# Performance work log

Hardware: AMD Instinct MI355X
Metric: run time of the kernel (lower is better)

The kernel has to match this reference:

```python
import jax, jax.numpy as jnp
import numpy as np

V, E, D_LAT, NC, L = 30000, 256, 256, 10, 4096
B = 8
D_IN = 2 * D_LAT   # mamba expand=2 -> 512
N_ST = 16          # d_state
DT_R = 16          # dt_rank = ceil(d_model/16)
D_CONV = 4


def conv1d(x, w, b, pad, groups=1):
    # x: [B,C,L], w: [O, C//groups, K] (torch layout)
    y = jax.lax.conv_general_dilated(x, w, (1,), [(pad[0], pad[1])],
                                     dimension_numbers=('NCH', 'OIH', 'NCH'),
                                     feature_group_count=groups)
    return y + b[None, :, None]


def setup_inputs() -> dict:
    key = jax.random.key(0)
    ks = jax.random.split(key, 12)
    nrm = lambda k, s, sc=0.02: (jax.random.normal(k, s) * sc).astype(jnp.float32)
    return {
        'tokens': jax.random.randint(ks[0], (B, L), 0, V),
        'emb': nrm(ks[1], (V, E)),
        'conv1_w': nrm(ks[2], (128, E, 5)), 'conv1_b': jnp.zeros((128,), jnp.float32),
        'conv2_w': nrm(ks[3], (D_LAT, 128, 3)), 'conv2_b': jnp.zeros((D_LAT,), jnp.float32),
        'in_proj_w': nrm(ks[4], (2 * D_IN, D_LAT)),
        'convdw_w': nrm(ks[5], (D_IN, 1, D_CONV), 0.2), 'convdw_b': jnp.zeros((D_IN,), jnp.float32),
        'x_proj_w': nrm(ks[6], (DT_R + 2 * N_ST, D_IN)),
        'dt_proj_w': nrm(ks[7], (D_IN, DT_R), 0.1),
        'dt_proj_b': jnp.full((D_IN,), -4.0, jnp.float32),  # softplus^-1 of small dt
        'A_log': jnp.broadcast_to(jnp.log(jnp.arange(1, N_ST + 1, dtype=jnp.float32)), (D_IN, N_ST)) + jnp.zeros((D_IN, N_ST), jnp.float32),
        'Dp': jnp.ones((D_IN,), jnp.float32),
        'out_proj_w': nrm(ks[8], (D_LAT, D_IN)),
        'fc_w': nrm(ks[9], (NC, D_LAT)), 'fc_b': jnp.zeros((NC,), jnp.float32),
    }


def mamba_block(u, in_proj_w, convdw_w, convdw_b, x_proj_w, dt_proj_w, dt_proj_b, A_log, Dp, out_proj_w):
    # u: [B, Lm, d_model]
    Bsz = u.shape[0]
    xz = u @ in_proj_w.T                              # [B,Lm,2*Din]
    x, z = jnp.split(xz, 2, axis=-1)
    # causal depthwise conv (torch pads both sides, slices [:L] == left-pad only)
    xc = conv1d(x.transpose(0, 2, 1), convdw_w, convdw_b, (D_CONV - 1, 0), groups=D_IN)
    x = jax.nn.silu(xc.transpose(0, 2, 1))            # [B,Lm,Din]
    dbc = x @ x_proj_w.T                              # [B,Lm,dt_rank+2N]
    dt, Bm, Cm = jnp.split(dbc, [DT_R, DT_R + N_ST], axis=-1)
    dt = jax.nn.softplus(dt @ dt_proj_w.T + dt_proj_b)  # [B,Lm,Din]
    A = -jnp.exp(A_log)                               # [Din,N]

    def step(h, inp):
        dt_t, B_t, C_t, x_t = inp                     # [B,Din],[B,N],[B,N],[B,Din]
        dA = jnp.exp(dt_t[..., None] * A)             # [B,Din,N]
        h = h * dA + (dt_t * x_t)[..., None] * B_t[:, None, :]
        y = jnp.einsum('bdn,bn->bd', h, C_t)
        return h, y

    h0 = jnp.zeros((Bsz, D_IN, N_ST), u.dtype)
    xs = (dt.transpose(1, 0, 2), Bm.transpose(1, 0, 2), Cm.transpose(1, 0, 2), x.transpose(1, 0, 2))
    _, ys = jax.lax.scan(step, h0, xs)                # [Lm,B,Din]
    y = ys.transpose(1, 0, 2) + x * Dp
    y = y * jax.nn.silu(z)
    return y @ out_proj_w.T                           # [B,Lm,d_model]


def reference(tokens, emb, conv1_w, conv1_b, conv2_w, conv2_b, in_proj_w, convdw_w, convdw_b,
              x_proj_w, dt_proj_w, dt_proj_b, A_log, Dp, out_proj_w, fc_w, fc_b):
    x = emb[tokens]                                   # [B,L,E]
    x = x.transpose(0, 2, 1)                          # [B,E,L]
    x = jax.nn.relu(conv1d(x, conv1_w, conv1_b, (2, 2)))
    b, c, l = x.shape
    x = x.reshape(b, c, l // 2, 2).max(-1)            # MaxPool1d(2)
    x = jax.nn.relu(conv1d(x, conv2_w, conv2_b, (1, 1)))
    x = x.transpose(0, 2, 1)                          # [B,L/2,latent]
    x = mamba_block(x, in_proj_w, convdw_w, convdw_b, x_proj_w, dt_proj_w, dt_proj_b, A_log, Dp, out_proj_w)
    x = x.mean(axis=1)                                # [B,latent]
    return x @ fc_w.T + fc_b                          # [B,num_classes]
```

## Files before the change

### kernel.cpp

```cpp
#include <hip/hip_runtime.h>
#include <hip/hip_bf16.h>

constexpr int Bn   = 8;
constexpr int L    = 4096;
constexpr int E    = 256;
constexpr int Lh   = 2048;
constexpr int C1n  = 128;
constexpr int Dlat = 256;
constexpr int Din  = 512;
constexpr int Nst  = 16;
constexpr int M2   = Bn * Lh;
constexpr int NCH  = 64;
constexpr int TC   = 32;

constexpr long o_wtx   = 0;
constexpr long o_wtdt  = o_wtx  + 512L*48;
constexpr long o_bf    = o_wtdt + 16L*512;
constexpr long o_xeb   = o_bf    + 524288/2;
constexpr long o_out1b = o_xeb   + (8L*4100*256)/2;
constexpr long o_ub    = o_out1b + (8L*2050*128)/2;
constexpr long o_xz    = o_ub    + (16384L*256)/2;
constexpr long o_xbuf  = o_xz    + 16384L*1024;
constexpr long o_dbc   = o_xbuf  + 16384L*512;
constexpr long o_dt    = o_dbc   + 16384L*48;
constexpr long o_hend  = o_dt    + 16384L*512;
constexpr long o_P     = o_hend  + 8L*512*NCH*16;
constexpr long o_hin   = o_P     + 8L*512*NCH*16;
constexpr long o_ym    = o_hin   + 8L*512*NCH*16;

typedef __attribute__((ext_vector_type(8))) short bf8_t;
typedef __attribute__((ext_vector_type(4))) float f4_t;

__device__ inline short f2bf(float f) {
    unsigned int u = __float_as_uint(f);
    unsigned int r = (u + 0x7FFFu + ((u >> 16) & 1u)) >> 16;
    return (short)r;
}

__global__ void k_prep(const float* __restrict__ w1, const float* __restrict__ w2,
                       const float* __restrict__ win, const float* __restrict__ xw,
                       const float* __restrict__ dtw, float* __restrict__ ws) {
    int idx = blockIdx.x * 256 + threadIdx.x;
    if (idx < 24576) {
        int n_ = idx % 48; int k = idx / 48;
        ws[o_wtx + idx] = xw[n_*512 + k];
    } else if (idx < 32768) {
        int j = idx - 24576;
        int n_ = j & 511; int k = j >> 9;
        ws[o_wtdt + j] = dtw[n_*16 + k];
    } else if (idx < 557056) {
        int j = idx - 32768;
        short* wsS = (short*)(ws + o_bf);
        if (j < 163840) {
            int n_ = j / 1280; int r = j - n_*1280; int s = r >> 8; int c = r & 255;
            wsS[j] = f2bf(w1[(n_*256 + c)*5 + s]);
        } else if (j < 262144) {
            int jj = j - 163840;
            int n_ = jj / 384; int r = jj - n_*384; int s = r >> 7; int c = r & 127;
            wsS[j] = f2bf(w2[(n_*128 + c)*3 + s]);
        } else {
            int jj = j - 262144;
            int n_ = jj >> 8; int k = jj & 255;
            wsS[j] = f2bf(win[n_*256 + k]);
        }
    }
}

__global__ void k_embed(const int* __restrict__ tok, const float* __restrict__ emb,
                        short* __restrict__ xeb) {
    int idx = blockIdx.x * 256 + threadIdx.x;
    int r = idx >> 5;
    int c8 = (idx & 31) << 3;
    int b = r / 4100; int tr = r - b*4100;
    bf8_t v = {0,0,0,0,0,0,0,0};
    if (tr >= 2 && tr < 4098) {
        int t = tok[b*4096 + tr - 2];
        const float* e = emb + (long)t*256 + c8;
        #pragma unroll
        for (int i = 0; i < 8; ++i) v[i] = f2bf(e[i]);
    }
    *(bf8_t*)&xeb[(long)r*256 + c8] = v;
}

__global__ void k_zpad(short* __restrict__ out1b) {
    int i = threadIdx.x;
    for (int j = i; j < 2048; j += 256) {
        int b = j >> 8; int rsel = (j >> 7) & 1; int c = j & 127;
        long row = (long)b*2050 + (rsel ? 2049 : 0);
        out1b[row*128 + c] = 0;
    }
}

template<int SHIFTS, int TPS, int EPI>
__global__ __launch_bounds__(256) void k_mgemm(const short* __restrict__ A, int ars, long batchA,
                                               const short* __restrict__ Bt, int ktot,
                                               const float* __restrict__ bias,
                                               short* __restrict__ outB, float* __restrict__ outF,
                                               int ors, long batchOut) {
    constexpr int KT = SHIFTS * TPS;
    constexpr int C  = TPS * 64;
    __shared__ short As[2][64][68];
    __shared__ short Bs[2][128][68];
    int tid = threadIdx.x;
    int l = tid & 63, w = tid >> 6;
    int m0 = blockIdx.x * 64;
    int n0 = blockIdx.y * 128;
    long zA = (long)blockIdx.z * batchA;
    long zO = (long)blockIdx.z * batchOut;

    bf8_t aReg[2], bReg[4];

    auto gload = [&](int kt) {
        int s = kt / TPS, c0 = (kt % TPS) * 64;
        const short* Ab = A + zA + (long)(m0 + s) * ars + c0;
        #pragma unroll
        for (int j = 0; j < 2; ++j) {
            int idx = tid + j*256;
            int r = idx >> 3, cc = (idx & 7) * 8;
            aReg[j] = *(const bf8_t*)&Ab[(long)r * ars + cc];
        }
        const short* Bb = Bt + (long)n0 * ktot + s * C + c0;
        #pragma unroll
        for (int j = 0; j < 4; ++j) {
            int idx = tid + j*256;
            int r = idx >> 3, cc = (idx & 7) * 8;
            bReg[j] = *(const bf8_t*)&Bb[(long)r * ktot + cc];
        }
    };
    auto lwrite = [&](int buf) {
        #pragma unroll
        for (int j = 0; j < 2; ++j) {
            int idx = tid + j*256;
            int r = idx >> 3, cc = (idx & 7) * 8;
            *(bf8_t*)&As[buf][r][cc] = aReg[j];
        }
        #pragma unroll
        for (int j = 0; j < 4; ++j) {
            int idx = tid + j*256;
            int r = idx >> 3, cc = (idx & 7) * 8;
            *(bf8_t*)&Bs[buf][r][cc] = bReg[j];
        }
    };

    f4_t acc[4][2];
    #pragma unroll
    for (int m = 0; m < 4; ++m)
        #pragma unroll
        for (int n = 0; n < 2; ++n) acc[m][n] = (f4_t){0.f, 0.f, 0.f, 0.f};

    gload(0);
    lwrite(0);
    __syncthreads();
    for (int kt = 0; kt < KT; ++kt) {
        int buf = kt & 1;
        if (kt + 1 < KT) gload(kt + 1);
        #pragma unroll
        for (int ks = 0; ks < 2; ++ks) {
            int kk = ks*32 + ((l >> 4) << 3);
            bf8_t a[4], b[2];
            #pragma unroll
            for (int m = 0; m < 4; ++m)
                a[m] = *(const bf8_t*)&As[buf][m*16 + (l & 15)][kk];
            #pragma unroll
            for (int n = 0; n < 2; ++n)
                b[n] = *(const bf8_t*)&Bs[buf][w*32 + n*16 + (l & 15)][kk];
            #pragma unroll
            for (int m = 0; m < 4; ++m)
                #pragma unroll
                for (int n = 0; n < 2; ++n)
                    acc[m][n] = __builtin_amdgcn_mfma_f32_16x16x32_bf16(a[m], b[n], acc[m][n], 0, 0, 0);
        }
        if (kt + 1 < KT) {
            lwrite(buf ^ 1);
            __syncthreads();
        }
    }

    #pragma unroll
    for (int mt = 0; mt < 4; ++mt)
        #pragma unroll
        for (int nt = 0; nt < 2; ++nt) {
            f4_t c = acc[mt][nt];
            int col = n0 + w*32 + nt*16 + (l & 15);
            int r0 = m0 + mt*16 + ((l >> 4) << 2);
            if constexpr (EPI == 0) {
                #pragma unroll
                for (int j = 0; j < 4; ++j)
                    outF[zO + (long)(r0 + j) * ors + col] = c[j];
            } else if constexpr (EPI == 1) {
                float bv = bias[col];
                #pragma unroll
                for (int j = 0; j < 4; ++j)
                    outB[zO + (long)(r0 + j) * ors + col] = f2bf(fmaxf(c[j] + bv, 0.f));
            } else {
                float bv = bias[col];
                float p0 = fmaxf(fmaxf(c[0], c[1]) + bv, 0.f);
                float p1 = fmaxf(fmaxf(c[2], c[3]) + bv, 0.f);
                int tp = r0 >> 1;
                outB[zO + (long)(tp + 1) * ors + col] = f2bf(p0);
                outB[zO + (long)(tp + 2) * ors + col] = f2bf(p1);
            }
        }
}

template<int ACT>
__global__ __launch_bounds__(256) void k_gemm(const float* __restrict__ A, int lda,
                                              const float* __restrict__ WT,
                                              const float* __restrict__ bias,
                                              float* __restrict__ out,
                                              int M, int N, int K) {
    __shared__ float As[16][68];
    __shared__ float Bs[16][64];
    int n0 = blockIdx.x * 64, m0 = blockIdx.y * 64;
    int tid = threadIdx.x;
    int ti = tid >> 4, tj = tid & 15;
    float acc[4][4] = {};
    for (int k0 = 0; k0 < K; k0 += 16) {
        {
            int mm = tid >> 2, kq = tid & 3;
            float4 v = *(const float4*)&A[(long)(m0 + mm)*lda + k0 + kq*4];
            As[kq*4+0][mm] = v.x; As[kq*4+1][mm] = v.y;
            As[kq*4+2][mm] = v.z; As[kq*4+3][mm] = v.w;
        }
        {
            int kk = tid >> 4, n4 = tid & 15;
            float4 v = {0.f,0.f,0.f,0.f};
            if (n0 + n4*4 < N)
                v = *(const float4*)&WT[(long)(k0 + kk)*N + n0 + n4*4];
            *(float4*)&Bs[kk][n4*4] = v;
        }
        __syncthreads();
        #pragma unroll
        for (int kk = 0; kk < 16; ++kk) {
            float4 av = *(float4*)&As[kk][ti*4];
            float4 bv = *(float4*)&Bs[kk][tj*4];
            acc[0][0] += av.x*bv.x; acc[0][1] += av.x*bv.y; acc[0][2] += av.x*bv.z; acc[0][3] += av.x*bv.w;
            acc[1][0] += av.y*bv.x; acc[1][1] += av.y*bv.y; acc[1][2] += av.y*bv.z; acc[1][3] += av.y*bv.w;
            acc[2][0] += av.z*bv.x; acc[2][1] += av.z*bv.y; acc[2][2] += av.z*bv.z; acc[2][3] += av.z*bv.w;
            acc[3][0] += av.w*bv.x; acc[3][1] += av.w*bv.y; acc[3][2] += av.w*bv.z; acc[3][3] += av.w*bv.w;
        }
        __syncthreads();
    }
    if (n0 + tj*4 >= N) return;
    float4 bv = {0.f,0.f,0.f,0.f};
    if (bias) bv = *(const float4*)&bias[n0 + tj*4];
    #pragma unroll
    for (int i = 0; i < 4; ++i) {
        int m = m0 + ti*4 + i;
        float4 v;
        v.x = acc[i][0] + bv.x; v.y = acc[i][1] + bv.y;
        v.z = acc[i][2] + bv.z; v.w = acc[i][3] + bv.w;
        if (ACT == 1) {
            v.x = (v.x > 20.f) ? v.x : log1pf(__expf(v.x));
            v.y = (v.y > 20.f) ? v.y : log1pf(__expf(v.y));
            v.z = (v.z > 20.f) ? v.z : log1pf(__expf(v.z));
            v.w = (v.w > 20.f) ? v.w : log1pf(__expf(v.w));
        }
        *(float4*)&out[(long)m*N + n0 + tj*4] = v;
    }
}

__global__ void k_dwconv(const float* __restrict__ xz, const float* __restrict__ wdw,
                         const float* __restrict__ bdw, float* __restrict__ xout) {
    int idx = blockIdx.x * 256 + threadIdx.x;
    int d4 = idx & 127; int rem = idx >> 7;
    int t = rem & 2047; int b = rem >> 11;
    int d0 = d4 * 4;
    float4 acc = *(const float4*)&bdw[d0];
    #pragma unroll
    for (int k = 0; k < 4; ++k) {
        int tt = t - 3 + k;
        if (tt >= 0) {
            float4 v = *(const float4*)&xz[((long)(b*Lh + tt))*1024 + d0];
            acc.x += v.x * wdw[(d0+0)*4 + k];
            acc.y += v.y * wdw[(d0+1)*4 + k];
            acc.z += v.z * wdw[(d0+2)*4 + k];
            acc.w += v.w * wdw[(d0+3)*4 + k];
        }
    }
    acc.x = acc.x / (1.f + __expf(-acc.x));
    acc.y = acc.y / (1.f + __expf(-acc.y));
    acc.z = acc.z / (1.f + __expf(-acc.z));
    acc.w = acc.w / (1.f + __expf(-acc.w));
    *(float4*)&xout[(long)idx * 4] = acc;
}

__global__ __launch_bounds__(256) void k_scan_a(const float* __restrict__ dt,
                                                const float* __restrict__ x,
                                                const float* __restrict__ dbc,
                                                const float* __restrict__ A_log,
                                                float* __restrict__ hend,
                                                float* __restrict__ Pbuf) {
    __shared__ float4 Bs4[TC][4];
    int c = blockIdx.x;
    int b = blockIdx.z;
    int tid = threadIdx.x;
    int d = blockIdx.y * 256 + tid;
    for (int i = tid; i < TC*4; i += 256) {
        int tt = i >> 2, q = i & 3;
        Bs4[tt][q] = *(const float4*)&dbc[((long)b*Lh + c*TC + tt)*48 + 16 + q*4];
    }
    __syncthreads();
    float A_[16];
    #pragma unroll
    for (int n = 0; n < 16; ++n) A_[n] = -__expf(A_log[d*16 + n]);
    float h[16];
    #pragma unroll
    for (int n = 0; n < 16; ++n) h[n] = 0.f;
    float sd = 0.f;
    long base = ((long)b*Lh + c*TC)*512 + d;
    #pragma unroll 4
    for (int tt = 0; tt < TC; ++tt) {
        float dtv = dt[base + (long)tt*512];
        float xv  = x[base + (long)tt*512];
        float u = dtv * xv;
        sd += dtv;
        float Bv[16];
        *(float4*)&Bv[0]  = Bs4[tt][0]; *(float4*)&Bv[4]  = Bs4[tt][1];
        *(float4*)&Bv[8]  = Bs4[tt][2]; *(float4*)&Bv[12] = Bs4[tt][3];
        #pragma unroll
        for (int n = 0; n < 16; ++n) {
            float dA = __expf(dtv * A_[n]);
            h[n] = h[n] * dA + u * Bv[n];
        }
    }
    long o = (((long)b*Din + d)*NCH + c)*16;
    #pragma unroll
    for (int n = 0; n < 16; ++n) hend[o + n] = h[n];
    #pragma unroll
    for (int n = 0; n < 16; ++n) Pbuf[o + n] = __expf(A_[n] * sd);
}

__global__ void k_scan_b(const float* __restrict__ hend, const float* __restrict__ Pbuf,
                         float* __restrict__ hin) {
    int idx = blockIdx.x * 256 + threadIdx.x;
    int n = idx & 15; long bd = idx >> 4;
    long base = bd * NCH * 16 + n;
    float h = 0.f;
    for (int c = 0; c < NCH; ++c) {
        hin[base + c*16] = h;
        h = hend[base + c*16] + Pbuf[base + c*16] * h;
    }
}

__global__ __launch_bounds__(256) void k_scan_c(const float* __restrict__ dt,
                                                const float* __restrict__ x,
                                                const float* __restrict__ xz,
                                                const float* __restrict__ dbc,
                                                const float* __restrict__ A_log,
                                                const float* __restrict__ Dp,
                                                const float* __restrict__ hin,
                                                float* __restrict__ ym) {
    __shared__ float4 Bs4[TC][4], Cs4[TC][4];
    int c = blockIdx.x;
    int b = blockIdx.z;
    int tid = threadIdx.x;
    int d = blockIdx.y * 256 + tid;
    for (int i = tid; i < TC*4; i += 256) {
        int tt = i >> 2, q = i & 3;
        long rb = ((long)b*Lh + c*TC + tt)*48;
        Bs4[tt][q] = *(const float4*)&dbc[rb + 16 + q*4];
        Cs4[tt][q] = *(const float4*)&dbc[rb + 32 + q*4];
    }
    __syncthreads();
    float A_[16];
    #pragma unroll
    for (int n = 0; n < 16; ++n) A_[n] = -__expf(A_log[d*16 + n]);
    float h[16];
    long o = (((long)b*Din + d)*NCH + c)*16;
    #pragma unroll
    for (int n = 0; n < 16; ++n) h[n] = hin[o + n];
    float Dpv = Dp[d];
    float ysum = 0.f;
    long base = ((long)b*Lh + c*TC)*512 + d;
    long zbase = ((long)b*Lh + c*TC)*1024 + 512 + d;
    #pragma unroll 2
    for (int tt = 0; tt < TC; ++tt) {
        float dtv = dt[base + (long)tt*512];
        float xv  = x[base + (long)tt*512];
        float zv  = xz[zbase + (long)tt*1024];
        float u = dtv * xv;
        float Bv[16], Cv[16];
        *(float4*)&Bv[0]  = Bs4[tt][0]; *(float4*)&Bv[4]  = Bs4[tt][1];
        *(float4*)&Bv[8]  = Bs4[tt][2]; *(float4*)&Bv[12] = Bs4[tt][3];
        *(float4*)&Cv[0]  = Cs4[tt][0]; *(float4*)&Cv[4]  = Cs4[tt][1];
        *(float4*)&Cv[8]  = Cs4[tt][2]; *(float4*)&Cv[12] = Cs4[tt][3];
        float p = 0.f;
        #pragma unroll
        for (int n = 0; n < 16; ++n) {
            float dA = __expf(dtv * A_[n]);
            h[n] = h[n] * dA + u * Bv[n];
            p += h[n] * Cv[n];
        }
        float sz = zv / (1.f + __expf(-zv));
        ysum += (p + xv * Dpv) * sz;
    }
    atomicAdd(&ym[b*Din + d], ysum);
}

__global__ void k_tail(const float* __restrict__ ym, const float* __restrict__ ow,
                       const float* __restrict__ fcw, const float* __restrict__ fcb,
                       float* __restrict__ out) {
    __shared__ float yls[512];
    __shared__ float xs[256];
    int b = blockIdx.x, c = threadIdx.x;
    yls[c] = ym[b*512 + c];
    yls[c + 256] = ym[b*512 + 256 + c];
    __syncthreads();
    float s = 0.f;
    for (int d = 0; d < 512; ++d) s += yls[d] * ow[c*512 + d];
    xs[c] = s * (1.f / 2048.f);
    __syncthreads();
    if (c < 10) {
        float t = fcb[c];
        for (int k = 0; k < 256; ++k) t += xs[k] * fcw[c*256 + k];
        out[b*10 + c] = t;
    }
}

extern "C" void kernel_launch(void* const* d_in, const int* in_sizes, int n_in,
                              void* d_out, int out_size, void* d_ws, size_t ws_size,
                              hipStream_t stream) {
    const int*   tok  = (const int*)d_in[0];
    const float* emb  = (const float*)d_in[1];
    const float* w1   = (const float*)d_in[2];
    const float* b1   = (const float*)d_in[3];
    const float* w2   = (const float*)d_in[4];
    const float* b2   = (const float*)d_in[5];
    const float* win  = (const float*)d_in[6];
    const float* wdw  = (const float*)d_in[7];
    const float* bdw  = (const float*)d_in[8];
    const float* xw   = (const float*)d_in[9];
    const float* dtw  = (const float*)d_in[10];
    const float* dtb  = (const float*)d_in[11];
    const float* alog = (const float*)d_in[12];
    const float* Dp   = (const float*)d_in[13];
    const float* ow   = (const float*)d_in[14];
    const float* fcw  = (const float*)d_in[15];
    const float* fcb  = (const float*)d_in[16];
    float* ws  = (float*)d_ws;
    float* out = (float*)d_out;

    float* wtx   = ws + o_wtx;
    float* wtdt  = ws + o_wtdt;
    short* wt1t  = (short*)(ws + o_bf);
    short* wt2t  = wt1t + 163840;
    short* wtint = wt2t + 98304;
    short* xeb   = (short*)(ws + o_xeb);
    short* out1b = (short*)(ws + o_out1b);
    short* ub    = (short*)(ws + o_ub);
    float* xz    = ws + o_xz;
    float* xbuf  = ws + o_xbuf;
    float* dbc   = ws + o_dbc;
    float* dtbuf = ws + o_dt;
    float* hend  = ws + o_hend;
    float* Pbuf  = ws + o_P;
    float* hin   = ws + o_hin;
    float* ym    = ws + o_ym;

    k_prep<<<2176, 256, 0, stream>>>(w1, w2, win, xw, dtw, ws);
    k_embed<<<4100, 256, 0, stream>>>(tok, emb, xeb);
    k_zpad<<<1, 256, 0, stream>>>(out1b);
    hipMemsetAsync(ym, 0, Bn*Din*sizeof(float), stream);
    k_mgemm<5, 4, 2><<<dim3(64, 1, 8), 256, 0, stream>>>(
        xeb, 256, 4100L*256, wt1t, 1280, b1, out1b, nullptr, 128, 2050L*128);
    k_mgemm<3, 2, 1><<<dim3(32, 2, 8), 256, 0, stream>>>(
        out1b, 128, 2050L*128, wt2t, 384, b2, ub, nullptr, 256, 2048L*256);
    k_mgemm<1, 4, 0><<<dim3(256, 8, 1), 256, 0, stream>>>(
        ub, 256, 0, wtint, 256, nullptr, nullptr, xz, 1024, 0);
    k_dwconv<<<(M2*128)/256, 256, 0, stream>>>(xz, wdw, bdw, xbuf);
    k_gemm<0><<<dim3(1, M2/64), 256, 0, stream>>>(xbuf, Din, wtx, nullptr, dbc, M2, 48, Din);
    k_gemm<1><<<dim3(8, M2/64), 256, 0, stream>>>(dbc, 48, wtdt, dtb, dtbuf, M2, 512, 16);
    k_scan_a<<<dim3(NCH, 2, Bn), 256, 0, stream>>>(dtbuf, xbuf, dbc, alog, hend, Pbuf);
    k_scan_b<<<(Bn*Din*Nst)/256, 256, 0, stream>>>(hend, Pbuf, hin);
    k_scan_c<<<dim3(NCH, 2, Bn), 256, 0, stream>>>(dtbuf, xbuf, xz, dbc, alog, Dp, hin, ym);
    k_tail<<<8, 256, 0, stream>>>(ym, ow, fcw, fcb, out);
}
```

Baseline: 413.5 us.

## Fold scan output into single pass with linear state correction; tile dwconv over time

The chunked selective scan now runs the full per-chunk recurrence only once. Each chunk computes its local output assuming zero initial state, plus a per-state weight S that captures how the incoming state contributes to the gated output sum. The second recurrence pass is replaced by a cheap dot product of S with the carried-in states, which removes a full re-read of dt/x/z and a second round of exponentials, and drops the atomics and the memset. Separately, the depthwise conv now computes four timesteps per thread with weights staged in shared memory, so overlapping inputs are reused. The cost is extra per-step multiplies for q and S and more intermediate buffers.

```diff
diff --git a/kernel.cpp b/kernel.cpp
--- a/kernel.cpp
+++ b/kernel.cpp
@@ -27,6 +27,8 @@
 constexpr long o_P     = o_hend  + 8L*512*NCH*16;
 constexpr long o_hin   = o_P     + 8L*512*NCH*16;
 constexpr long o_ym    = o_hin   + 8L*512*NCH*16;
+constexpr long o_S     = o_ym    + 8L*512;
+constexpr long o_yp    = o_S     + 8L*512*NCH*16;
 
 typedef __attribute__((ext_vector_type(8))) short bf8_t;
 typedef __attribute__((ext_vector_type(4))) float f4_t;
@@ -260,97 +262,67 @@
     }
 }
 
-__global__ void k_dwconv(const float* __restrict__ xz, const float* __restrict__ wdw,
-                         const float* __restrict__ bdw, float* __restrict__ xout) {
-    int idx = blockIdx.x * 256 + threadIdx.x;
-    int d4 = idx & 127; int rem = idx >> 7;
-    int t = rem & 2047; int b = rem >> 11;
+__global__ __launch_bounds__(256) void k_dwconv(const float* __restrict__ xz,
+                                                const float* __restrict__ wdw,
+                                                const float* __restrict__ bdw,
+                                                float* __restrict__ xout) {
+    __shared__ float wk[4][512];
+    __shared__ float bs[512];
+    int tid = threadIdx.x;
+    for (int e = tid; e < 2048; e += 256) {
+        int k = e >> 9, d = e & 511;
+        wk[k][d] = wdw[d*4 + k];
+    }
+    bs[tid] = bdw[tid];
+    bs[tid + 256] = bdw[tid + 256];
+    __syncthreads();
+
+    int idx = blockIdx.x * 256 + tid;
+    int d4 = idx & 127;
+    int tg = (idx >> 7) & 511;
+    int b  = idx >> 16;
     int d0 = d4 * 4;
-    float4 acc = *(const float4*)&bdw[d0];
-    #pragma unroll
-    for (int k = 0; k < 4; ++k) {
-        int tt = t - 3 + k;
-        if (tt >= 0) {
-            float4 v = *(const float4*)&xz[((long)(b*Lh + tt))*1024 + d0];
-            acc.x += v.x * wdw[(d0+0)*4 + k];
-            acc.y += v.y * wdw[(d0+1)*4 + k];
-            acc.z += v.z * wdw[(d0+2)*4 + k];
-            acc.w += v.w * wdw[(d0+3)*4 + k];
-        }
-    }
-    acc.x = acc.x / (1.f + __expf(-acc.x));
-    acc.y = acc.y / (1.f + __expf(-acc.y));
-    acc.z = acc.z / (1.f + __expf(-acc.z));
-    acc.w = acc.w / (1.f + __expf(-acc.w));
-    *(float4*)&xout[(long)idx * 4] = acc;
+    int t0 = tg * 4;
+
+    float4 x[7];
+    #pragma unroll
+    for (int i = 0; i < 7; ++i) {
+        int t = t0 - 3 + i;
+        x[i] = (t >= 0) ? *(const float4*)&xz[((long)(b*Lh + t))*1024 + d0]
+                        : (float4){0.f, 0.f, 0.f, 0.f};
+    }
+    float4 w[4];
+    #pragma unroll
+    for (int k = 0; k < 4; ++k) w[k] = *(float4*)&wk[k][d0];
+    float4 bias4 = *(float4*)&bs[d0];
+
+    #pragma unroll
+    for (int j = 0; j < 4; ++j) {
+        float4 a = bias4;
+        #pragma unroll
+        for (int k = 0; k < 4; ++k) {
+            float4 v = x[j + k];
+            a.x += v.x * w[k].x; a.y += v.y * w[k].y;
+            a.z += v.z * w[k].z; a.w += v.w * w[k].w;
+        }
+        a.x = a.x / (1.f + __expf(-a.x));
+        a.y = a.y / (1.f + __expf(-a.y));
+        a.z = a.z / (1.f + __expf(-a.z));
+        a.w = a.w / (1.f + __expf(-a.w));
+        *(float4*)&xout[((long)(b*Lh + t0 + j))*512 + d0] = a;
+    }
 }
 
 __global__ __launch_bounds__(256) void k_scan_a(const float* __restrict__ dt,
-                                                const float* __restrict__ x,
-                                                const float* __restrict__ dbc,
-                                                const float* __restrict__ A_log,
-                                                float* __restrict__ hend,
-                                                float* __restrict__ Pbuf) {
-    __shared__ float4 Bs4[TC][4];
-    int c = blockIdx.x;
-    int b = blockIdx.z;
-    int tid = threadIdx.x;
-    int d = blockIdx.y * 256 + tid;
-    for (int i = tid; i < TC*4; i += 256) {
-        int tt = i >> 2, q = i & 3;
-        Bs4[tt][q] = *(const float4*)&dbc[((long)b*Lh + c*TC + tt)*48 + 16 + q*4];
-    }
-    __syncthreads();
-    float A_[16];
-    #pragma unroll
-    for (int n = 0; n < 16; ++n) A_[n] = -__expf(A_log[d*16 + n]);
-    float h[16];
-    #pragma unroll
-    for (int n = 0; n < 16; ++n) h[n] = 0.f;
-    float sd = 0.f;
-    long base = ((long)b*Lh + c*TC)*512 + d;
-    #pragma unroll 4
-    for (int tt = 0; tt < TC; ++tt) {
-        float dtv = dt[base + (long)tt*512];
-        float xv  = x[base + (long)tt*512];
-        float u = dtv * xv;
-        sd += dtv;
-        float Bv[16];
-        *(float4*)&Bv[0]  = Bs4[tt][0]; *(float4*)&Bv[4]  = Bs4[tt][1];
-        *(float4*)&Bv[8]  = Bs4[tt][2]; *(float4*)&Bv[12] = Bs4[tt][3];
-        #pragma unroll
-        for (int n = 0; n < 16; ++n) {
-            float dA = __expf(dtv * A_[n]);
-            h[n] = h[n] * dA + u * Bv[n];
-        }
-    }
-    long o = (((long)b*Din + d)*NCH + c)*16;
-    #pragma unroll
-    for (int n = 0; n < 16; ++n) hend[o + n] = h[n];
-    #pragma unroll
-    for (int n = 0; n < 16; ++n) Pbuf[o + n] = __expf(A_[n] * sd);
-}
-
-__global__ void k_scan_b(const float* __restrict__ hend, const float* __restrict__ Pbuf,
-                         float* __restrict__ hin) {
-    int idx = blockIdx.x * 256 + threadIdx.x;
-    int n = idx & 15; long bd = idx >> 4;
-    long base = bd * NCH * 16 + n;
-    float h = 0.f;
-    for (int c = 0; c < NCH; ++c) {
-        hin[base + c*16] = h;
-        h = hend[base + c*16] + Pbuf[base + c*16] * h;
-    }
-}
-
-__global__ __launch_bounds__(256) void k_scan_c(const float* __restrict__ dt,
                                                 const float* __restrict__ x,
                                                 const float* __restrict__ xz,
                                                 const float* __restrict__ dbc,
                                                 const float* __restrict__ A_log,
                                                 const float* __restrict__ Dp,
-                                                const float* __restrict__ hin,
-                                                float* __restrict__ ym) {
+                                                float* __restrict__ hend,
+                                                float* __restrict__ Pbuf,
+                                                float* __restrict__ Sbuf,
+                                                float* __restrict__ ypart) {
     __shared__ float4 Bs4[TC][4], Cs4[TC][4];
     int c = blockIdx.x;
     int b = blockIdx.z;
@@ -366,20 +338,19 @@
     float A_[16];
     #pragma unroll
     for (int n = 0; n < 16; ++n) A_[n] = -__expf(A_log[d*16 + n]);
-    float h[16];
-    long o = (((long)b*Din + d)*NCH + c)*16;
-    #pragma unroll
-    for (int n = 0; n < 16; ++n) h[n] = hin[o + n];
+    float h[16], q[16], S[16];
+    #pragma unroll
+    for (int n = 0; n < 16; ++n) { h[n] = 0.f; q[n] = 1.f; S[n] = 0.f; }
     float Dpv = Dp[d];
-    float ysum = 0.f;
-    long base = ((long)b*Lh + c*TC)*512 + d;
+    float yp = 0.f;
+    long base  = ((long)b*Lh + c*TC)*512 + d;
     long zbase = ((long)b*Lh + c*TC)*1024 + 512 + d;
-    #pragma unroll 2
     for (int tt = 0; tt < TC; ++tt) {
         float dtv = dt[base + (long)tt*512];
         float xv  = x[base + (long)tt*512];
         float zv  = xz[zbase + (long)tt*1024];
         float u = dtv * xv;
+        float gate = zv / (1.f + __expf(-zv));
         float Bv[16], Cv[16];
         *(float4*)&Bv[0]  = Bs4[tt][0]; *(float4*)&Bv[4]  = Bs4[tt][1];
         *(float4*)&Bv[8]  = Bs4[tt][2]; *(float4*)&Bv[12] = Bs4[tt][3];
@@ -390,12 +361,56 @@
         for (int n = 0; n < 16; ++n) {
             float dA = __expf(dtv * A_[n]);
             h[n] = h[n] * dA + u * Bv[n];
+            q[n] *= dA;
             p += h[n] * Cv[n];
-        }
-        float sz = zv / (1.f + __expf(-zv));
-        ysum += (p + xv * Dpv) * sz;
-    }
-    atomicAdd(&ym[b*Din + d], ysum);
+            S[n] += (gate * Cv[n]) * q[n];
+        }
+        yp += gate * (p + xv * Dpv);
+    }
+    long o = (((long)b*Din + d)*NCH + c)*16;
+    #pragma unroll
+    for (int n = 0; n < 16; ++n) hend[o + n] = h[n];
+    #pragma unroll
+    for (int n = 0; n < 16; ++n) Pbuf[o + n] = q[n];
+    #pragma unroll
+    for (int n = 0; n < 16; ++n) Sbuf[o + n] = S[n];
+    ypart[((long)b*Din + d)*NCH + c] = yp;
+}
+
+__global__ void k_scan_b(const float* __restrict__ hend, const float* __restrict__ Pbuf,
+                         float* __restrict__ hin) {
+    int idx = blockIdx.x * 256 + threadIdx.x;
+    int n = idx & 15; long bd = idx >> 4;
+    long base = bd * NCH * 16 + n;
+    float h = 0.f;
+    for (int c = 0; c < NCH; ++c) {
+        hin[base + c*16] = h;
+        h = hend[base + c*16] + Pbuf[base + c*16] * h;
+    }
+}
+
+__global__ __launch_bounds__(256) void k_scan_cl(const float* __restrict__ Sbuf,
+                                                 const float* __restrict__ hin,
+                                                 const float* __restrict__ ypart,
+                                                 float* __restrict__ ym) {
+    int idx = blockIdx.x * 256 + threadIdx.x;
+    int c = idx & 63;
+    long bd = idx >> 6;
+    long o = (bd * NCH + c) * 16;
+    float v = ypart[bd * NCH + c];
+    #pragma unroll
+    for (int qq = 0; qq < 4; ++qq) {
+        float4 s = *(const float4*)&Sbuf[o + qq*4];
+        float4 hi = *(const float4*)&hin[o + qq*4];
+        v += s.x*hi.x + s.y*hi.y + s.z*hi.z + s.w*hi.w;
+    }
+    v += __shfl_xor(v, 1);
+    v += __shfl_xor(v, 2);
+    v += __shfl_xor(v, 4);
+    v += __shfl_xor(v, 8);
+    v += __shfl_xor(v, 16);
+    v += __shfl_xor(v, 32);
+    if (c == 0) ym[bd] = v;
 }
 
 __global__ void k_tail(const float* __restrict__ ym, const float* __restrict__ ow,
@@ -457,22 +472,24 @@
     float* Pbuf  = ws + o_P;
     float* hin   = ws + o_hin;
     float* ym    = ws + o_ym;
+    float* Sbuf  = ws + o_S;
+    float* ypart = ws + o_yp;
 
     k_prep<<<2176, 256, 0, stream>>>(w1, w2, win, xw, dtw, ws);
     k_embed<<<4100, 256, 0, stream>>>(tok, emb, xeb);
     k_zpad<<<1, 256, 0, stream>>>(out1b);
-    hipMemsetAsync(ym, 0, Bn*Din*sizeof(float), stream);
     k_mgemm<5, 4, 2><<<dim3(64, 1, 8), 256, 0, stream>>>(
         xeb, 256, 4100L*256, wt1t, 1280, b1, out1b, nullptr, 128, 2050L*128);
     k_mgemm<3, 2, 1><<<dim3(32, 2, 8), 256, 0, stream>>>(
         out1b, 128, 2050L*128, wt2t, 384, b2, ub, nullptr, 256, 2048L*256);
     k_mgemm<1, 4, 0><<<dim3(256, 8, 1), 256, 0, stream>>>(
         ub, 256, 0, wtint, 256, nullptr, nullptr, xz, 1024, 0);
-    k_dwconv<<<(M2*128)/256, 256, 0, stream>>>(xz, wdw, bdw, xbuf);
+    k_dwconv<<<2048, 256, 0, stream>>>(xz, wdw, bdw, xbuf);
     k_gemm<0><<<dim3(1, M2/64), 256, 0, stream>>>(xbuf, Din, wtx, nullptr, dbc, M2, 48, Din);
     k_gemm<1><<<dim3(8, M2/64), 256, 0, stream>>>(dbc, 48, wtdt, dtb, dtbuf, M2, 512, 16);
-    k_scan_a<<<dim3(NCH, 2, Bn), 256, 0, stream>>>(dtbuf, xbuf, dbc, alog, hend, Pbuf);
+    k_scan_a<<<dim3(NCH, 2, Bn), 256, 0, stream>>>(dtbuf, xbuf, xz, dbc, alog, Dp,
+                                                   hend, Pbuf, Sbuf, ypart);
     k_scan_b<<<(Bn*Din*Nst)/256, 256, 0, stream>>>(hend, Pbuf, hin);
-    k_scan_c<<<dim3(NCH, 2, Bn), 256, 0, stream>>>(dtbuf, xbuf, xz, dbc, alog, Dp, hin, ym);
+    k_scan_cl<<<(Bn*Din*NCH)/256, 256, 0, stream>>>(Sbuf, hin, ypart, ym);
     k_tail<<<8, 256, 0, stream>>>(ym, ow, fcw, fcb, out);
 }
```

Measured after the change: 353.9 us. 14.4% less time.
